# Kernel tuning notes

Hardware: AMD Instinct MI355X
Metric: run time of the kernel (lower is better)

The kernel has to match this reference:

```python
import jax, jax.numpy as jnp
import numpy as np

B = 8192          # batch
NS = 2048         # no_of_states -> state width = 2*NS = 4096
NH = 1024         # no_of_heads  -> action width and output width
HID = 512         # hidden_size (fixed in module)
INPUT = NS * 2 + 4 + NH   # 5124, context_input width


def _layer(key, fan_in, fan_out):
    # matches torch nn.Linear default init: U(-1/sqrt(fan_in), 1/sqrt(fan_in))
    kw, kb = jax.random.split(key)
    bound = 1.0 / np.sqrt(fan_in)
    W = jax.random.uniform(kw, (fan_in, fan_out), minval=-bound, maxval=bound, dtype=jnp.float32)
    b = jax.random.uniform(kb, (fan_out,), minval=-bound, maxval=bound, dtype=jnp.float32)
    return W, b


def setup_inputs() -> dict:
    key = jax.random.key(0)
    keys = jax.random.split(key, 20)
    inp = {
        'state': jax.random.normal(keys[0], (B, NS * 2), dtype=jnp.float32),
        'action': jax.random.normal(keys[1], (B, NH), dtype=jnp.float32),
        'task_indicator': jax.random.normal(keys[2], (B, 4), dtype=jnp.float32),
    }
    specs = [
        ('cx1_1', 4, HID * 2), ('cx1_2', HID * 2, HID * 2),
        ('cx2_1', 4, HID * 2), ('cx2_2', HID * 2, HID * 2),
        ('cx3_1', 4, HID),     ('cx3_2', HID, HID),
        ('cx4_1', 4, NH),      ('cx4_2', NH, NH),
        ('l1', INPUT, HID * 4),
        ('l2', HID * 4 + INPUT, HID * 2),
        ('l3', HID * 2 + INPUT, HID * 2),
        ('l4', HID * 2 + INPUT, HID),
        ('l5', HID, NH),
    ]
    for i, (name, fi, fo) in enumerate(specs):
        W, b = _layer(keys[3 + i], fi, fo)
        inp['W_' + name] = W
        inp['b_' + name] = b
    return inp


def _kwta(x, k_winners):
    # Faithful to the original: top-k values are scattered back to their own
    # indices and non-top-k entries are left untouched -> identity map.
    return x


def reference(state, action, task_indicator,
              W_cx1_1, b_cx1_1, W_cx1_2, b_cx1_2,
              W_cx2_1, b_cx2_1, W_cx2_2, b_cx2_2,
              W_cx3_1, b_cx3_1, W_cx3_2, b_cx3_2,
              W_cx4_1, b_cx4_1, W_cx4_2, b_cx4_2,
              W_l1, b_l1, W_l2, b_l2, W_l3, b_l3, W_l4, b_l4, W_l5, b_l5):
    ctx = jnp.concatenate([state, task_indicator, action], axis=1)  # [B, INPUT]

    # context (k-winner-count) branches; mathematically dead wrt output
    cx1 = jnp.tanh(task_indicator @ W_cx1_1 + b_cx1_1) @ W_cx1_2 + b_cx1_2
    cx2 = jnp.tanh(task_indicator @ W_cx2_1 + b_cx2_1) @ W_cx2_2 + b_cx2_2
    cx3 = jnp.tanh(task_indicator @ W_cx3_1 + b_cx3_1) @ W_cx3_2 + b_cx3_2
    cx4 = jnp.tanh(task_indicator @ W_cx4_1 + b_cx4_1) @ W_cx4_2 + b_cx4_2

    x = ctx @ W_l1 + b_l1                       # [B, 2048]
    x = _kwta(x, cx1)
    x = jnp.concatenate([x, ctx], axis=1)       # [B, 2048+INPUT]
    x = x @ W_l2 + b_l2                         # [B, 1024]
    x = _kwta(x, cx2)
    x = jnp.concatenate([x, ctx], axis=1)
    x = x @ W_l3 + b_l3                         # [B, 1024]
    x = _kwta(x, cx3)
    x = jnp.concatenate([x, ctx], axis=1)
    x = x @ W_l4 + b_l4                         # [B, 512]
    x = _kwta(x, cx4)
    out = x @ W_l5 + b_l5                       # [B, NH]
    return out
```

## Files before the change

kernel.cpp:

```cpp
#include <hip/hip_runtime.h>
#include <hip/hip_bf16.h>
#include <stdint.h>

#define B_ROWS   8192
#define CTX_REAL 5124
#define CTX_PAD  5184

typedef unsigned short u16;
typedef __attribute__((ext_vector_type(8))) short short8;
typedef __attribute__((ext_vector_type(4))) float f32x4;

#define AS1 __attribute__((address_space(1)))
#define AS3 __attribute__((address_space(3)))

__device__ __forceinline__ u16 f2bf(float f) {
    union { float f; uint32_t u; } v; v.f = f;
    uint32_t u = v.u;
    uint32_t r = 0x7fffu + ((u >> 16) & 1u);
    return (u16)((u + r) >> 16);
}

__global__ void build_ctx(const float* __restrict__ state,
                          const float* __restrict__ ti,
                          const float* __restrict__ action,
                          u16* __restrict__ ctx) {
    const int row = blockIdx.y;
    const int c2  = blockIdx.x * blockDim.x + threadIdx.x;
    const int col = c2 * 2;
    if (col >= CTX_PAD) return;

    float v0, v1;
    {
        int c = col;
        v0 = (c < 4096) ? state[(size_t)row * 4096 + c]
           : (c < 4100) ? ti[(size_t)row * 4 + (c - 4096)]
           : (c < 5124) ? action[(size_t)row * 1024 + (c - 4100)]
           : 0.0f;
        c = col + 1;
        v1 = (c < 4096) ? state[(size_t)row * 4096 + c]
           : (c < 4100) ? ti[(size_t)row * 4 + (c - 4096)]
           : (c < 5124) ? action[(size_t)row * 1024 + (c - 4100)]
           : 0.0f;
    }
    uint32_t packed = (uint32_t)f2bf(v0) | ((uint32_t)f2bf(v1) << 16);
    *(uint32_t*)&ctx[(size_t)row * CTX_PAD + col] = packed;
}

__global__ void wconv(const float* __restrict__ W, u16* __restrict__ Wt,
                      int K_real, int Kpad, int N) {
    __shared__ float tile[64][65];
    const int k0 = blockIdx.x * 64;
    const int n0 = blockIdx.y * 64;
    const int t  = threadIdx.x;
#pragma unroll
    for (int i = 0; i < 16; ++i) {
        int idx = i * 256 + t;
        int r = idx >> 6, c = idx & 63;
        int k = k0 + r;
        tile[r][c] = (k < K_real) ? W[(size_t)k * N + n0 + c] : 0.0f;
    }
    __syncthreads();
#pragma unroll
    for (int i = 0; i < 16; ++i) {
        int idx = i * 256 + t;
        int rn = idx >> 6, ck = idx & 63;
        Wt[(size_t)(n0 + rn) * Kpad + k0 + ck] = f2bf(tile[ck][rn]);
    }
}

template <int TM, int TN, int MW, int NW, bool OUT_BF16>
__global__ __launch_bounds__(256, 2)
void gemm_bias(const u16* __restrict__ A1, int lda1, int K1,
               const u16* __restrict__ A2, int lda2,
               const u16* __restrict__ Bt, int ldb, int Ktot,
               const float* __restrict__ bias,
               void* __restrict__ Cout, int ldc) {
    constexpr int FI = TM / MW / 16;
    constexpr int FJ = TN / NW / 16;
    __shared__ u16 tA[TM * 64];
    __shared__ u16 tB[TN * 64];

    const int t    = threadIdx.x;
    const int wave = t >> 6;
    const int lane = t & 63;
    const int quad = lane >> 4;
    const int l16  = lane & 15;
    const int wr   = (wave / NW) * (TM / MW);
    const int wc   = (wave % NW) * (TN / NW);
    const int rowBase = blockIdx.x * TM;
    const int colBase = blockIdx.y * TN;

    const int srow = t >> 3;
    const int scol = ((t & 7) ^ (srow & 7)) * 8;

    const u16* gA1 = A1 + (size_t)(rowBase + srow) * lda1 + scol;
    const u16* gA2 = A2 ? (A2 + (size_t)(rowBase + srow) * lda2 + scol) : gA1;
    const u16* gB  = Bt + (size_t)(colBase + srow) * ldb + scol;

    char* ldsA = (char*)tA + wave * 1024;
    char* ldsB = (char*)tB + wave * 1024;

    f32x4 acc[FI][FJ] = {};

    const int nKt = Ktot >> 6;
    for (int kt = 0; kt < nKt; ++kt) {
        const int k0 = kt << 6;
        const u16* srcA;
        int strideA;
        if (k0 < K1) { srcA = gA1 + k0;        strideA = lda1; }
        else         { srcA = gA2 + (k0 - K1); strideA = lda2; }
        const u16* srcB = gB + k0;

        __syncthreads();
#pragma unroll
        for (int it = 0; it < TM / 32; ++it)
            __builtin_amdgcn_global_load_lds(
                (AS1 const void*)(srcA + (size_t)(it * 32) * strideA),
                (AS3 void*)(ldsA + it * 4096), 16, 0, 0);
#pragma unroll
        for (int it = 0; it < TN / 32; ++it)
            __builtin_amdgcn_global_load_lds(
                (AS1 const void*)(srcB + (size_t)(it * 32) * ldb),
                (AS3 void*)(ldsB + it * 4096), 16, 0, 0);
        __syncthreads();

        const u16* tAw = tA + wr * 64;
        const u16* tBw = tB + wc * 64;
#pragma unroll
        for (int kk = 0; kk < 2; ++kk) {
            const int kchunk = kk * 4 + quad;
            const int swz    = (kchunk ^ (l16 & 7)) * 8;
            short8 a[FI], b[FJ];
#pragma unroll
            for (int i = 0; i < FI; ++i)
                a[i] = *(const short8*)(tAw + (i * 16 + l16) * 64 + swz);
#pragma unroll
            for (int j = 0; j < FJ; ++j)
                b[j] = *(const short8*)(tBw + (j * 16 + l16) * 64 + swz);
#pragma unroll
            for (int i = 0; i < FI; ++i)
#pragma unroll
                for (int j = 0; j < FJ; ++j)
                    acc[i][j] = __builtin_amdgcn_mfma_f32_16x16x32_bf16(
                        a[i], b[j], acc[i][j], 0, 0, 0);
        }
    }

    if (OUT_BF16) {
        u16* C = (u16*)Cout;
#pragma unroll
        for (int i = 0; i < FI; ++i) {
            const int r0 = rowBase + wr + i * 16 + quad * 4;
#pragma unroll
            for (int j = 0; j < FJ; ++j) {
                const int c = colBase + wc + j * 16 + l16;
                const float bb = bias[c];
#pragma unroll
                for (int r = 0; r < 4; ++r)
                    C[(size_t)(r0 + r) * ldc + c] = f2bf(acc[i][j][r] + bb);
            }
        }
    } else {
        float* C = (float*)Cout;
#pragma unroll
        for (int i = 0; i < FI; ++i) {
            const int r0 = rowBase + wr + i * 16 + quad * 4;
#pragma unroll
            for (int j = 0; j < FJ; ++j) {
                const int c = colBase + wc + j * 16 + l16;
                const float bb = bias[c];
#pragma unroll
                for (int r = 0; r < 4; ++r)
                    C[(size_t)(r0 + r) * ldc + c] = acc[i][j][r] + bb;
            }
        }
    }
}

extern "C" void kernel_launch(void* const* d_in, const int* in_sizes, int n_in,
                              void* d_out, int out_size, void* d_ws, size_t ws_size,
                              hipStream_t stream) {
    const float* state  = (const float*)d_in[0];
    const float* action = (const float*)d_in[1];
    const float* ti     = (const float*)d_in[2];
    const float* W_l1 = (const float*)d_in[19]; const float* b_l1 = (const float*)d_in[20];
    const float* W_l2 = (const float*)d_in[21]; const float* b_l2 = (const float*)d_in[22];
    const float* W_l3 = (const float*)d_in[23]; const float* b_l3 = (const float*)d_in[24];
    const float* W_l4 = (const float*)d_in[25]; const float* b_l4 = (const float*)d_in[26];
    const float* W_l5 = (const float*)d_in[27]; const float* b_l5 = (const float*)d_in[28];

    char* ws = (char*)d_ws;
    size_t off = 0;
    auto alloc = [&](size_t bytes) -> void* {
        void* p = ws + off;
        off += (bytes + 255) & ~(size_t)255;
        return p;
    };
    u16* ctx = (u16*)alloc((size_t)B_ROWS * CTX_PAD * 2);
    u16* x1  = (u16*)alloc((size_t)B_ROWS * 2048 * 2);
    u16* x2  = (u16*)alloc((size_t)B_ROWS * 1024 * 2);
    u16* x3  = (u16*)alloc((size_t)B_ROWS * 1024 * 2);
    u16* x4  = (u16*)alloc((size_t)B_ROWS * 512 * 2);
    u16* W1t = (u16*)alloc((size_t)2048 * 5184 * 2);
    u16* W2t = (u16*)alloc((size_t)1024 * 7232 * 2);
    u16* W3t = (u16*)alloc((size_t)1024 * 6208 * 2);
    u16* W4t = (u16*)alloc((size_t)512  * 6208 * 2);
    u16* W5t = (u16*)alloc((size_t)1024 * 512  * 2);

    build_ctx<<<dim3((CTX_PAD / 2 + 255) / 256, B_ROWS), 256, 0, stream>>>(state, ti, action, ctx);
    wconv<<<dim3(81, 32),  256, 0, stream>>>(W_l1, W1t, 5124, 5184, 2048);
    wconv<<<dim3(113, 16), 256, 0, stream>>>(W_l2, W2t, 7172, 7232, 1024);
    wconv<<<dim3(97, 16),  256, 0, stream>>>(W_l3, W3t, 6148, 6208, 1024);
    wconv<<<dim3(97, 8),   256, 0, stream>>>(W_l4, W4t, 6148, 6208, 512);
    wconv<<<dim3(8, 16),   256, 0, stream>>>(W_l5, W5t, 512, 512, 1024);

    gemm_bias<256, 128, 4, 1, true><<<dim3(32, 16), 256, 0, stream>>>(
        ctx, CTX_PAD, CTX_PAD, nullptr, 0, W1t, 5184, 5184, b_l1, x1, 2048);
    gemm_bias<256, 128, 4, 1, true><<<dim3(32, 8), 256, 0, stream>>>(
        x1, 2048, 2048, ctx, CTX_PAD, W2t, 7232, 7232, b_l2, x2, 1024);
    gemm_bias<256, 128, 4, 1, true><<<dim3(32, 8), 256, 0, stream>>>(
        x2, 1024, 1024, ctx, CTX_PAD, W3t, 6208, 6208, b_l3, x3, 1024);
    gemm_bias<128, 128, 2, 2, true><<<dim3(64, 4), 256, 0, stream>>>(
        x3, 1024, 1024, ctx, CTX_PAD, W4t, 6208, 6208, b_l4, x4, 512);
    gemm_bias<128, 128, 2, 2, false><<<dim3(64, 8), 256, 0, stream>>>(
        x4, 512, 512, nullptr, 0, W5t, 512, 512, b_l5, d_out, 1024);
}
```

Measured before the change: 975.6 us.

## Switch GEMM to 32x32x16 bf16 MFMA and retile layers 2-3

The GEMM inner loop now issues 32x32x16 bf16 MFMA instructions instead of 16x16x32. Each wave handles larger 32x32 output fragments with 16-register accumulators, and the fragment loads and swizzle plus the epilogue row mapping are reworked to match. Layers 2 and 3 also move to 128x128 tiles on a 2x2 wave grid, which launches more blocks. The larger MFMA reads fewer LDS bytes per FLOP. In exchange, each block reuses less data from its tiles, and the epilogue writes strided rows.

```diff
diff --git a/kernel.cpp b/kernel.cpp
--- a/kernel.cpp
+++ b/kernel.cpp
@@ -8,7 +8,7 @@
 
 typedef unsigned short u16;
 typedef __attribute__((ext_vector_type(8))) short short8;
-typedef __attribute__((ext_vector_type(4))) float f32x4;
+typedef __attribute__((ext_vector_type(16))) float f32x16;
 
 #define AS1 __attribute__((address_space(1)))
 #define AS3 __attribute__((address_space(3)))
@@ -75,16 +75,17 @@
                const u16* __restrict__ Bt, int ldb, int Ktot,
                const float* __restrict__ bias,
                void* __restrict__ Cout, int ldc) {
-    constexpr int FI = TM / MW / 16;
-    constexpr int FJ = TN / NW / 16;
+    constexpr int FI = TM / MW / 32;
+    constexpr int FJ = TN / NW / 32;
     __shared__ u16 tA[TM * 64];
     __shared__ u16 tB[TN * 64];
 
     const int t    = threadIdx.x;
     const int wave = t >> 6;
     const int lane = t & 63;
-    const int quad = lane >> 4;
-    const int l16  = lane & 15;
+    const int l32  = lane & 31;
+    const int half = lane >> 5;
+    const int lswz = lane & 7;
     const int wr   = (wave / NW) * (TM / MW);
     const int wc   = (wave % NW) * (TN / NW);
     const int rowBase = blockIdx.x * TM;
@@ -100,7 +101,7 @@
     char* ldsA = (char*)tA + wave * 1024;
     char* ldsB = (char*)tB + wave * 1024;
 
-    f32x4 acc[FI][FJ] = {};
+    f32x16 acc[FI][FJ] = {};
 
     const int nKt = Ktot >> 6;
     for (int kt = 0; kt < nKt; ++kt) {
@@ -127,21 +128,21 @@
         const u16* tAw = tA + wr * 64;
         const u16* tBw = tB + wc * 64;
 #pragma unroll
-        for (int kk = 0; kk < 2; ++kk) {
-            const int kchunk = kk * 4 + quad;
-            const int swz    = (kchunk ^ (l16 & 7)) * 8;
+        for (int ks = 0; ks < 4; ++ks) {
+            const int kchunk = ks * 2 + half;
+            const int swz    = (kchunk ^ lswz) * 8;
             short8 a[FI], b[FJ];
 #pragma unroll
             for (int i = 0; i < FI; ++i)
-                a[i] = *(const short8*)(tAw + (i * 16 + l16) * 64 + swz);
+                a[i] = *(const short8*)(tAw + (i * 32 + l32) * 64 + swz);
 #pragma unroll
             for (int j = 0; j < FJ; ++j)
-                b[j] = *(const short8*)(tBw + (j * 16 + l16) * 64 + swz);
+                b[j] = *(const short8*)(tBw + (j * 32 + l32) * 64 + swz);
 #pragma unroll
             for (int i = 0; i < FI; ++i)
 #pragma unroll
                 for (int j = 0; j < FJ; ++j)
-                    acc[i][j] = __builtin_amdgcn_mfma_f32_16x16x32_bf16(
+                    acc[i][j] = __builtin_amdgcn_mfma_f32_32x32x16_bf16(
                         a[i], b[j], acc[i][j], 0, 0, 0);
         }
     }
@@ -150,28 +151,32 @@
         u16* C = (u16*)Cout;
 #pragma unroll
         for (int i = 0; i < FI; ++i) {
-            const int r0 = rowBase + wr + i * 16 + quad * 4;
+            const int rbase = rowBase + wr + i * 32 + 4 * half;
 #pragma unroll
             for (int j = 0; j < FJ; ++j) {
-                const int c = colBase + wc + j * 16 + l16;
+                const int c = colBase + wc + j * 32 + l32;
                 const float bb = bias[c];
 #pragma unroll
-                for (int r = 0; r < 4; ++r)
-                    C[(size_t)(r0 + r) * ldc + c] = f2bf(acc[i][j][r] + bb);
+                for (int reg = 0; reg < 16; ++reg) {
+                    const int r = rbase + (reg & 3) + 8 * (reg >> 2);
+                    C[(size_t)r * ldc + c] = f2bf(acc[i][j][reg] + bb);
+                }
             }
         }
     } else {
         float* C = (float*)Cout;
 #pragma unroll
         for (int i = 0; i < FI; ++i) {
-            const int r0 = rowBase + wr + i * 16 + quad * 4;
+            const int rbase = rowBase + wr + i * 32 + 4 * half;
 #pragma unroll
             for (int j = 0; j < FJ; ++j) {
-                const int c = colBase + wc + j * 16 + l16;
+                const int c = colBase + wc + j * 32 + l32;
                 const float bb = bias[c];
 #pragma unroll
-                for (int r = 0; r < 4; ++r)
-                    C[(size_t)(r0 + r) * ldc + c] = acc[i][j][r] + bb;
+                for (int reg = 0; reg < 16; ++reg) {
+                    const int r = rbase + (reg & 3) + 8 * (reg >> 2);
+                    C[(size_t)r * ldc + c] = acc[i][j][reg] + bb;
+                }
             }
         }
     }
@@ -216,9 +221,9 @@
 
     gemm_bias<256, 128, 4, 1, true><<<dim3(32, 16), 256, 0, stream>>>(
         ctx, CTX_PAD, CTX_PAD, nullptr, 0, W1t, 5184, 5184, b_l1, x1, 2048);
-    gemm_bias<256, 128, 4, 1, true><<<dim3(32, 8), 256, 0, stream>>>(
+    gemm_bias<128, 128, 2, 2, true><<<dim3(64, 8), 256, 0, stream>>>(
         x1, 2048, 2048, ctx, CTX_PAD, W2t, 7232, 7232, b_l2, x2, 1024);
-    gemm_bias<256, 128, 4, 1, true><<<dim3(32, 8), 256, 0, stream>>>(
+    gemm_bias<128, 128, 2, 2, true><<<dim3(64, 8), 256, 0, stream>>>(
         x2, 1024, 1024, ctx, CTX_PAD, W3t, 6208, 6208, b_l3, x3, 1024);
     gemm_bias<128, 128, 2, 2, true><<<dim3(64, 4), 256, 0, stream>>>(
         x3, 1024, 1024, ctx, CTX_PAD, W4t, 6208, 6208, b_l4, x4, 512);
```

Result: faster. 944.6 us (-3.2%).
